# Optimization experiments

Hardware: AMD Instinct MI355X
Metric: run time of the kernel (lower is better)

The kernel has to match this reference:

```python
import jax, jax.numpy as jnp
import numpy as np

N, T, H, E = 16384, 4, 64, 262144
NEG_SLOPE = 0.2  # LeakyReLU slope for GAT-style attention
LN_EPS = 1e-5


def setup_inputs() -> dict:
    key = jax.random.key(0)
    ks = jax.random.split(key, 24)
    p = {}
    p["pred"] = jax.random.normal(ks[0], (N, T, H), jnp.float32)
    p["ei_structural"] = jax.random.randint(ks[1], (2, E), 0, N, jnp.int32)
    p["ei_functional"] = jax.random.randint(ks[2], (2, E), 0, N, jnp.int32)
    scale = 1.0 / np.sqrt(H)
    i = 3
    for l in range(2):
        for et in ("s", "f"):
            p[f"W{l}{et}"] = (jax.random.normal(ks[i], (H, H), jnp.float32) * scale); i += 1
            p[f"a{l}{et}"] = (jax.random.normal(ks[i], (H,), jnp.float32) * scale); i += 1
        p[f"g{l}"] = jnp.ones((H,), jnp.float32)
        p[f"b{l}"] = jnp.zeros((H,), jnp.float32)
    return p


def _conv(x, ei, W, a, n_dst):
    """Attention-based ST graph conv, temporal_kernel_size=1 (per-step)."""
    h = jnp.einsum('nth,hd->ntd', x, W)          # [N,T,H] linear transform
    src, dst = ei[0], ei[1]
    he = h[src]                                   # [E,T,H] gather per edge
    logits = jax.nn.leaky_relu(jnp.einsum('eth,h->et', he, a), NEG_SLOPE)
    m = jax.ops.segment_max(logits, dst, num_segments=n_dst)     # [N,T]
    ex = jnp.exp(logits - m[dst])                 # stable softmax over incoming edges
    den = jax.ops.segment_sum(ex, dst, num_segments=n_dst)
    alpha = ex / den[dst]                         # [E,T]
    return jax.ops.segment_sum(alpha[..., None] * he, dst, num_segments=n_dst)


def _ln(x, g, b):
    mu = x.mean(-1, keepdims=True)
    v = x.var(-1, keepdims=True)
    return (x - mu) * jax.lax.rsqrt(v + LN_EPS) * g + b


def reference(pred, ei_structural, ei_functional,
              W0s, a0s, W0f, a0f, g0, b0,
              W1s, a1s, W1f, a1f, g1, b1):
    x = pred
    layers = ((W0s, a0s, W0f, a0f, g0, b0), (W1s, a1s, W1f, a1f, g1, b1))
    for (Ws, av, Wf, af, g, b) in layers:
        ms = _conv(x, ei_structural, Ws, av, N)
        mf = _conv(x, ei_functional, Wf, af, N)
        # sum(messages)/len(messages), residual, LayerNorm over H (dropout=identity in eval)
        x = _ln(x + 0.5 * (ms + mf), g, b)
    return x
```

## Files before the change

### kernel.cpp

```cpp
#include <hip/hip_runtime.h>
#include <hip/hip_bf16.h>

#define NN 16384
#define TT 4
#define HH 64
#define NT (NN * TT)
#define CAP 128
#define NEG_SLOPE 0.2f
#define LN_EPS 1e-5f

typedef __attribute__((ext_vector_type(8))) short short8;
typedef __attribute__((ext_vector_type(4))) float f32x4;

__device__ __forceinline__ float bf2f(unsigned short u) {
    return __uint_as_float((unsigned)u << 16);
}
__device__ __forceinline__ unsigned short f2bf(float f) {
    unsigned u = __float_as_uint(f);
    return (unsigned short)((u + 0x7FFF + ((u >> 16) & 1)) >> 16);
}


__global__ void zero_kernel(int* __restrict__ a, int n) {
    int i = blockIdx.x * blockDim.x + threadIdx.x;
    if (i < n) a[i] = 0;
}

__global__ void scatter_bucket_kernel(const int* __restrict__ ei_s, const int* __restrict__ ei_f,
                                      int* __restrict__ cnt2, int* __restrict__ col2, int E) {
    int e = blockIdx.x * blockDim.x + threadIdx.x;
    if (e < E) {
        int d = ei_s[E + e];
        int pos = atomicAdd(&cnt2[d], 1);
        if (pos < CAP) col2[d * CAP + pos] = ei_s[e];
    } else {
        e -= E;
        if (e < E) {
            int d = ei_f[E + e];
            int pos = atomicAdd(&cnt2[NN + d], 1);
            if (pos < CAP) col2[(long)NN * CAP + d * CAP + pos] = ei_f[e];
        }
    }
}


__global__ __launch_bounds__(256) void transform2_kernel(
    const float4* __restrict__ x4,
    const float* __restrict__ Ws, const float* __restrict__ as_,
    const float* __restrict__ Wf, const float* __restrict__ af,
    unsigned short* __restrict__ h_s, float* __restrict__ esc_s,
    unsigned short* __restrict__ h_f, float* __restrict__ esc_f) {
    const int lane = threadIdx.x & 63;
    const int wv = threadIdx.x >> 6;
    const int m = lane & 15;
    const int quad = lane >> 4;

    short8 Bs[4][2], Bf[4][2];
#pragma unroll
    for (int c = 0; c < 4; c++) {
#pragma unroll
        for (int ks = 0; ks < 2; ks++) {
#pragma unroll
            for (int j = 0; j < 8; j++) {
                int k = ks * 32 + quad * 8 + j;
                int n = c * 16 + m;
                Bs[c][ks][j] = (short)f2bf(Ws[k * 64 + n]);
                Bf[c][ks][j] = (short)f2bf(Wf[k * 64 + n]);
            }
        }
    }
    float a_s[4], a_f[4];
#pragma unroll
    for (int c = 0; c < 4; c++) { a_s[c] = as_[c * 16 + m]; a_f[c] = af[c * 16 + m]; }

    const int rowbase = blockIdx.x * 128 + wv * 32;
#pragma unroll
    for (int rt = 0; rt < 2; rt++) {
        const int row0 = rowbase + rt * 16;
        const long xbase = (long)(row0 + m) * 16 + quad * 2;
        float4 xa = x4[xbase];
        float4 xb = x4[xbase + 1];
        float4 xc = x4[xbase + 8];
        float4 xd = x4[xbase + 9];
        short8 A0, A1;
        A0[0] = (short)f2bf(xa.x); A0[1] = (short)f2bf(xa.y);
        A0[2] = (short)f2bf(xa.z); A0[3] = (short)f2bf(xa.w);
        A0[4] = (short)f2bf(xb.x); A0[5] = (short)f2bf(xb.y);
        A0[6] = (short)f2bf(xb.z); A0[7] = (short)f2bf(xb.w);
        A1[0] = (short)f2bf(xc.x); A1[1] = (short)f2bf(xc.y);
        A1[2] = (short)f2bf(xc.z); A1[3] = (short)f2bf(xc.w);
        A1[4] = (short)f2bf(xd.x); A1[5] = (short)f2bf(xd.y);
        A1[6] = (short)f2bf(xd.z); A1[7] = (short)f2bf(xd.w);

        f32x4 accs[4], accf[4];
#pragma unroll
        for (int c = 0; c < 4; c++) {
            accs[c] = (f32x4){0.f, 0.f, 0.f, 0.f};
            accf[c] = (f32x4){0.f, 0.f, 0.f, 0.f};
        }
#pragma unroll
        for (int c = 0; c < 4; c++) {
            accs[c] = __builtin_amdgcn_mfma_f32_16x16x32_bf16(A0, Bs[c][0], accs[c], 0, 0, 0);
            accs[c] = __builtin_amdgcn_mfma_f32_16x16x32_bf16(A1, Bs[c][1], accs[c], 0, 0, 0);
            accf[c] = __builtin_amdgcn_mfma_f32_16x16x32_bf16(A0, Bf[c][0], accf[c], 0, 0, 0);
            accf[c] = __builtin_amdgcn_mfma_f32_16x16x32_bf16(A1, Bf[c][1], accf[c], 0, 0, 0);
        }
#pragma unroll
        for (int reg = 0; reg < 4; reg++) {
            const int row = row0 + quad * 4 + reg;
            float ps = 0.f, pf = 0.f;
#pragma unroll
            for (int c = 0; c < 4; c++) {
                h_s[(long)row * 64 + c * 16 + m] = f2bf(accs[c][reg]);
                h_f[(long)row * 64 + c * 16 + m] = f2bf(accf[c][reg]);
                ps = fmaf(accs[c][reg], a_s[c], ps);
                pf = fmaf(accf[c][reg], a_f[c], pf);
            }
#pragma unroll
            for (int off = 1; off < 16; off <<= 1) {
                ps += __shfl_xor(ps, off, 64);
                pf += __shfl_xor(pf, off, 64);
            }
            if (m == 0) {
                float ls = (ps > 0.f) ? ps : NEG_SLOPE * ps;
                float lf = (pf > 0.f) ? pf : NEG_SLOPE * pf;
                esc_s[row] = __expf(ls);
                esc_f[row] = __expf(lf);
            }
        }
    }
}


__global__ __launch_bounds__(256) void aggregate_kernel(
    const float4* __restrict__ x4,
    const ushort4* __restrict__ hs4, const float* __restrict__ escs,
    const int* __restrict__ cnts, const int* __restrict__ cols,
    const ushort4* __restrict__ hf4, const float* __restrict__ escf,
    const int* __restrict__ cntf, const int* __restrict__ colf,
    const float4* __restrict__ g4, const float4* __restrict__ b4,
    float4* __restrict__ out4) {
    const int wv = threadIdx.x >> 6;
    const int lane = threadIdx.x & 63;
    const int n = blockIdx.x * 4 + wv;
    const int t = lane >> 4;
    const int ci = lane & 15;

    int cS = cnts[n]; if (cS > CAP) cS = CAP;
    int cF = cntf[n]; if (cF > CAP) cF = CAP;
    const int* colS = cols + (long)n * CAP;
    const int* colF = colf + (long)n * CAP;

    float dS = 0.f, sx = 0.f, sy = 0.f, sz = 0.f, sw = 0.f;
    float dF = 0.f, fx = 0.f, fy = 0.f, fz = 0.f, fw = 0.f;

    const int nbS = (cS + 3) >> 2;
    const int nbF = (cF + 3) >> 2;
    const int nb = nbS > nbF ? nbS : nbF;

    for (int it = 0; it < nb; ++it) {
        const int j = it << 2;
        const bool doS = it < nbS;
        const bool doF = it < nbF;
        int sS[4], sF[4];
        float eS[4], eF[4];
        ushort4 hS[4], hF[4];

        if (doS) {
#pragma unroll
            for (int u = 0; u < 4; u++) { int idx = j + u; sS[u] = colS[idx < cS ? idx : cS - 1]; }
        }
        if (doF) {
#pragma unroll
            for (int u = 0; u < 4; u++) { int idx = j + u; sF[u] = colF[idx < cF ? idx : cF - 1]; }
        }
        if (doS) {
#pragma unroll
            for (int u = 0; u < 4; u++) { float e = escs[sS[u] * 4 + t]; eS[u] = (j + u < cS) ? e : 0.f; }
#pragma unroll
            for (int u = 0; u < 4; u++) hS[u] = hs4[(long)sS[u] * 64 + lane];
        }
        if (doF) {
#pragma unroll
            for (int u = 0; u < 4; u++) { float e = escf[sF[u] * 4 + t]; eF[u] = (j + u < cF) ? e : 0.f; }
#pragma unroll
            for (int u = 0; u < 4; u++) hF[u] = hf4[(long)sF[u] * 64 + lane];
        }
        if (doS) {
#pragma unroll
            for (int u = 0; u < 4; u++) {
                dS += eS[u];
                sx = fmaf(eS[u], bf2f(hS[u].x), sx);
                sy = fmaf(eS[u], bf2f(hS[u].y), sy);
                sz = fmaf(eS[u], bf2f(hS[u].z), sz);
                sw = fmaf(eS[u], bf2f(hS[u].w), sw);
            }
        }
        if (doF) {
#pragma unroll
            for (int u = 0; u < 4; u++) {
                dF += eF[u];
                fx = fmaf(eF[u], bf2f(hF[u].x), fx);
                fy = fmaf(eF[u], bf2f(hF[u].y), fy);
                fz = fmaf(eF[u], bf2f(hF[u].z), fz);
                fw = fmaf(eF[u], bf2f(hF[u].w), fw);
            }
        }
    }

    float msx = 0.f, msy = 0.f, msz = 0.f, msw = 0.f;
    if (dS > 0.f) {
        float r = 1.f / dS;
        msx = sx * r; msy = sy * r; msz = sz * r; msw = sw * r;
    }
    float mfx = 0.f, mfy = 0.f, mfz = 0.f, mfw = 0.f;
    if (dF > 0.f) {
        float r = 1.f / dF;
        mfx = fx * r; mfy = fy * r; mfz = fz * r; mfw = fw * r;
    }

    float4 xv = x4[(long)n * 64 + lane];
    float v0 = xv.x + 0.5f * (msx + mfx);
    float v1 = xv.y + 0.5f * (msy + mfy);
    float v2 = xv.z + 0.5f * (msz + mfz);
    float v3 = xv.w + 0.5f * (msw + mfw);

    float sum = (v0 + v1) + (v2 + v3);
#pragma unroll
    for (int off = 1; off < 16; off <<= 1) sum += __shfl_xor(sum, off, 64);
    float mu = sum * (1.f / 64.f);
    float d0 = v0 - mu, d1 = v1 - mu, d2 = v2 - mu, d3 = v3 - mu;
    float var = (d0 * d0 + d1 * d1) + (d2 * d2 + d3 * d3);
#pragma unroll
    for (int off = 1; off < 16; off <<= 1) var += __shfl_xor(var, off, 64);
    var *= (1.f / 64.f);
    float inv = rsqrtf(var + LN_EPS);
    float4 gv = g4[ci], bv = b4[ci];
    float4 o;
    o.x = d0 * inv * gv.x + bv.x;
    o.y = d1 * inv * gv.y + bv.y;
    o.z = d2 * inv * gv.z + bv.z;
    o.w = d3 * inv * gv.w + bv.w;
    out4[(long)n * 64 + lane] = o;
}


extern "C" void kernel_launch(void* const* d_in, const int* in_sizes, int n_in,
                              void* d_out, int out_size, void* d_ws, size_t ws_size,
                              hipStream_t stream) {
    const float* pred = (const float*)d_in[0];
    const int* ei_s = (const int*)d_in[1];
    const int* ei_f = (const int*)d_in[2];
    const float* W0s = (const float*)d_in[3];
    const float* a0s = (const float*)d_in[4];
    const float* W0f = (const float*)d_in[5];
    const float* a0f = (const float*)d_in[6];
    const float* g0  = (const float*)d_in[7];
    const float* b0  = (const float*)d_in[8];
    const float* W1s = (const float*)d_in[9];
    const float* a1s = (const float*)d_in[10];
    const float* W1f = (const float*)d_in[11];
    const float* a1f = (const float*)d_in[12];
    const float* g1  = (const float*)d_in[13];
    const float* b1  = (const float*)d_in[14];
    const int E = in_sizes[1] / 2;

    char* ws = (char*)d_ws;
    auto alloc = [&](size_t bytes) {
        char* p = ws;
        ws += (bytes + 255) & ~(size_t)255;
        return p;
    };
    int* cnt2 = (int*)alloc((size_t)2 * NN * sizeof(int));
    int* col2 = (int*)alloc((size_t)2 * NN * CAP * sizeof(int));
    unsigned short* h_s = (unsigned short*)alloc((size_t)NT * HH * sizeof(unsigned short));
    unsigned short* h_f = (unsigned short*)alloc((size_t)NT * HH * sizeof(unsigned short));
    float* esc_s = (float*)alloc((size_t)NT * sizeof(float));
    float* esc_f = (float*)alloc((size_t)NT * sizeof(float));
    float* x_mid = (float*)alloc((size_t)NT * HH * sizeof(float));

    const int* cnt_s = cnt2;
    const int* cnt_f = cnt2 + NN;
    const int* col_s = col2;
    const int* col_f = col2 + (size_t)NN * CAP;

    const int EB = (E + 255) / 256;

    zero_kernel<<<(2 * NN) / 256, 256, 0, stream>>>(cnt2, 2 * NN);
    scatter_bucket_kernel<<<2 * EB, 256, 0, stream>>>(ei_s, ei_f, cnt2, col2, E);

    transform2_kernel<<<NT / 128, 256, 0, stream>>>(
        (const float4*)pred, W0s, a0s, W0f, a0f, h_s, esc_s, h_f, esc_f);
    aggregate_kernel<<<NN / 4, 256, 0, stream>>>(
        (const float4*)pred, (const ushort4*)h_s, esc_s, cnt_s, col_s,
        (const ushort4*)h_f, esc_f, cnt_f, col_f,
        (const float4*)g0, (const float4*)b0, (float4*)x_mid);

    transform2_kernel<<<NT / 128, 256, 0, stream>>>(
        (const float4*)x_mid, W1s, a1s, W1f, a1f, h_s, esc_s, h_f, esc_f);
    aggregate_kernel<<<NN / 4, 256, 0, stream>>>(
        (const float4*)x_mid, (const ushort4*)h_s, esc_s, cnt_s, col_s,
        (const ushort4*)h_f, esc_f, cnt_f, col_f,
        (const float4*)g1, (const float4*)b1, (float4*)d_out);
}
```

Measured before the change: 227.5 us.

## Split neighbor buckets by source half, preload indices per lane, prepack weights

Edge buckets are split four ways (edge type × source-node half) with a capacity of 64 each. The aggregate kernel loads one wave-wide vector of neighbor indices per bucket and broadcasts them with readlane, instead of issuing scalar column loads inside the loop. Gathers are unrolled by 8 and grouped so each phase touches only half of the h table, which may improve cache locality. Weights are also converted to bf16 MFMA fragments once in a small prepack kernel rather than in every transform block. The trade-off is an extra launch, more count and column storage, and a tighter per-bucket cap that could drop edges for skewed graphs.

```diff
diff --git a/kernel.cpp b/kernel.cpp
--- a/kernel.cpp
+++ b/kernel.cpp
@@ -5,7 +5,7 @@
 #define TT 4
 #define HH 64
 #define NT (NN * TT)
-#define CAP 128
+#define CAPH 64
 #define NEG_SLOPE 0.2f
 #define LN_EPS 1e-5f
 
@@ -26,28 +26,51 @@
     if (i < n) a[i] = 0;
 }
 
-__global__ void scatter_bucket_kernel(const int* __restrict__ ei_s, const int* __restrict__ ei_f,
-                                      int* __restrict__ cnt2, int* __restrict__ col2, int E) {
+__global__ void scatter4_kernel(const int* __restrict__ ei_s, const int* __restrict__ ei_f,
+                                int* __restrict__ cnt4, int* __restrict__ col4, int E) {
     int e = blockIdx.x * blockDim.x + threadIdx.x;
+    int src, d, set;
     if (e < E) {
-        int d = ei_s[E + e];
-        int pos = atomicAdd(&cnt2[d], 1);
-        if (pos < CAP) col2[d * CAP + pos] = ei_s[e];
+        set = 0; src = ei_s[e]; d = ei_s[E + e];
     } else {
         e -= E;
-        if (e < E) {
-            int d = ei_f[E + e];
-            int pos = atomicAdd(&cnt2[NN + d], 1);
-            if (pos < CAP) col2[(long)NN * CAP + d * CAP + pos] = ei_f[e];
-        }
-    }
+        if (e >= E) return;
+        set = 1; src = ei_f[e]; d = ei_f[E + e];
+    }
+    int half = src >> 13;
+    int p = set * 2 + half;
+    int pos = atomicAdd(&cnt4[p * NN + d], 1);
+    if (pos < CAPH) col4[((long)p * NN + d) * CAPH + pos] = src;
+}
+
+
+__global__ __launch_bounds__(256) void packw_kernel(
+    const float* __restrict__ W0s_, const float* __restrict__ W0f_,
+    const float* __restrict__ W1s_, const float* __restrict__ W1f_,
+    short8* __restrict__ wpack) {
+    int id = blockIdx.x * 256 + threadIdx.x;
+    int mat = id >> 9;
+    int slot = id & 511;
+    int lane = slot & 63;
+    int cks = slot >> 6;
+    int c = cks >> 1, ks = cks & 1;
+    int m = lane & 15, quad = lane >> 4;
+    const float* W = (mat == 0) ? W0s_ : (mat == 1) ? W0f_ : (mat == 2) ? W1s_ : W1f_;
+    short8 v;
+#pragma unroll
+    for (int j = 0; j < 8; j++) {
+        int k = ks * 32 + quad * 8 + j;
+        int n = c * 16 + m;
+        v[j] = (short)f2bf(W[k * 64 + n]);
+    }
+    wpack[id] = v;
 }
 
 
 __global__ __launch_bounds__(256) void transform2_kernel(
     const float4* __restrict__ x4,
-    const float* __restrict__ Ws, const float* __restrict__ as_,
-    const float* __restrict__ Wf, const float* __restrict__ af,
+    const short8* __restrict__ wp_s, const float* __restrict__ as_,
+    const short8* __restrict__ wp_f, const float* __restrict__ af,
     unsigned short* __restrict__ h_s, float* __restrict__ esc_s,
     unsigned short* __restrict__ h_f, float* __restrict__ esc_f) {
     const int lane = threadIdx.x & 63;
@@ -60,13 +83,8 @@
     for (int c = 0; c < 4; c++) {
 #pragma unroll
         for (int ks = 0; ks < 2; ks++) {
-#pragma unroll
-            for (int j = 0; j < 8; j++) {
-                int k = ks * 32 + quad * 8 + j;
-                int n = c * 16 + m;
-                Bs[c][ks][j] = (short)f2bf(Ws[k * 64 + n]);
-                Bf[c][ks][j] = (short)f2bf(Wf[k * 64 + n]);
-            }
+            Bs[c][ks] = wp_s[(c * 2 + ks) * 64 + lane];
+            Bf[c][ks] = wp_f[(c * 2 + ks) * 64 + lane];
         }
     }
     float a_s[4], a_f[4];
@@ -132,12 +150,40 @@
 }
 
 
+__device__ __forceinline__ void agg_phase(const ushort4* __restrict__ h4,
+                                          const float* __restrict__ esc,
+                                          int idx, int c, int t, int lane,
+                                          float& den, float& ax, float& ay,
+                                          float& az, float& aw) {
+    const int nb = (c + 7) >> 3;
+    for (int it = 0; it < nb; ++it) {
+        const int j = it << 3;
+        int s[8];
+        float e[8];
+        ushort4 h[8];
+#pragma unroll
+        for (int u = 0; u < 8; u++) s[u] = __builtin_amdgcn_readlane(idx, j + u);
+#pragma unroll
+        for (int u = 0; u < 8; u++) h[u] = h4[s[u] * 64 + lane];
+#pragma unroll
+        for (int u = 0; u < 8; u++) e[u] = esc[s[u] * 4 + t];
+#pragma unroll
+        for (int u = 0; u < 8; u++) {
+            float w = (j + u < c) ? e[u] : 0.f;
+            den += w;
+            ax = fmaf(w, bf2f(h[u].x), ax);
+            ay = fmaf(w, bf2f(h[u].y), ay);
+            az = fmaf(w, bf2f(h[u].z), az);
+            aw = fmaf(w, bf2f(h[u].w), aw);
+        }
+    }
+}
+
 __global__ __launch_bounds__(256) void aggregate_kernel(
     const float4* __restrict__ x4,
     const ushort4* __restrict__ hs4, const float* __restrict__ escs,
-    const int* __restrict__ cnts, const int* __restrict__ cols,
     const ushort4* __restrict__ hf4, const float* __restrict__ escf,
-    const int* __restrict__ cntf, const int* __restrict__ colf,
+    const int* __restrict__ cnt4, const int* __restrict__ col4,
     const float4* __restrict__ g4, const float4* __restrict__ b4,
     float4* __restrict__ out4) {
     const int wv = threadIdx.x >> 6;
@@ -146,67 +192,23 @@
     const int t = lane >> 4;
     const int ci = lane & 15;
 
-    int cS = cnts[n]; if (cS > CAP) cS = CAP;
-    int cF = cntf[n]; if (cF > CAP) cF = CAP;
-    const int* colS = cols + (long)n * CAP;
-    const int* colF = colf + (long)n * CAP;
+    int cc[4], idx[4];
+#pragma unroll
+    for (int p = 0; p < 4; p++) {
+        int cv = cnt4[p * NN + n];
+        if (cv > CAPH) cv = CAPH;
+        cc[p] = __builtin_amdgcn_readfirstlane(cv);
+        idx[p] = col4[((long)p * NN + n) * CAPH + lane];
+        if (lane >= cc[p]) idx[p] = 0;
+    }
 
     float dS = 0.f, sx = 0.f, sy = 0.f, sz = 0.f, sw = 0.f;
     float dF = 0.f, fx = 0.f, fy = 0.f, fz = 0.f, fw = 0.f;
 
-    const int nbS = (cS + 3) >> 2;
-    const int nbF = (cF + 3) >> 2;
-    const int nb = nbS > nbF ? nbS : nbF;
-
-    for (int it = 0; it < nb; ++it) {
-        const int j = it << 2;
-        const bool doS = it < nbS;
-        const bool doF = it < nbF;
-        int sS[4], sF[4];
-        float eS[4], eF[4];
-        ushort4 hS[4], hF[4];
-
-        if (doS) {
-#pragma unroll
-            for (int u = 0; u < 4; u++) { int idx = j + u; sS[u] = colS[idx < cS ? idx : cS - 1]; }
-        }
-        if (doF) {
-#pragma unroll
-            for (int u = 0; u < 4; u++) { int idx = j + u; sF[u] = colF[idx < cF ? idx : cF - 1]; }
-        }
-        if (doS) {
-#pragma unroll
-            for (int u = 0; u < 4; u++) { float e = escs[sS[u] * 4 + t]; eS[u] = (j + u < cS) ? e : 0.f; }
-#pragma unroll
-            for (int u = 0; u < 4; u++) hS[u] = hs4[(long)sS[u] * 64 + lane];
-        }
-        if (doF) {
-#pragma unroll
-            for (int u = 0; u < 4; u++) { float e = escf[sF[u] * 4 + t]; eF[u] = (j + u < cF) ? e : 0.f; }
-#pragma unroll
-            for (int u = 0; u < 4; u++) hF[u] = hf4[(long)sF[u] * 64 + lane];
-        }
-        if (doS) {
-#pragma unroll
-            for (int u = 0; u < 4; u++) {
-                dS += eS[u];
-                sx = fmaf(eS[u], bf2f(hS[u].x), sx);
-                sy = fmaf(eS[u], bf2f(hS[u].y), sy);
-                sz = fmaf(eS[u], bf2f(hS[u].z), sz);
-                sw = fmaf(eS[u], bf2f(hS[u].w), sw);
-            }
-        }
-        if (doF) {
-#pragma unroll
-            for (int u = 0; u < 4; u++) {
-                dF += eF[u];
-                fx = fmaf(eF[u], bf2f(hF[u].x), fx);
-                fy = fmaf(eF[u], bf2f(hF[u].y), fy);
-                fz = fmaf(eF[u], bf2f(hF[u].z), fz);
-                fw = fmaf(eF[u], bf2f(hF[u].w), fw);
-            }
-        }
-    }
+    agg_phase(hs4, escs, idx[0], cc[0], t, lane, dS, sx, sy, sz, sw);
+    agg_phase(hs4, escs, idx[1], cc[1], t, lane, dS, sx, sy, sz, sw);
+    agg_phase(hf4, escf, idx[2], cc[2], t, lane, dF, fx, fy, fz, fw);
+    agg_phase(hf4, escf, idx[3], cc[3], t, lane, dF, fx, fy, fz, fw);
 
     float msx = 0.f, msy = 0.f, msz = 0.f, msw = 0.f;
     if (dS > 0.f) {
@@ -271,35 +273,33 @@
         ws += (bytes + 255) & ~(size_t)255;
         return p;
     };
-    int* cnt2 = (int*)alloc((size_t)2 * NN * sizeof(int));
-    int* col2 = (int*)alloc((size_t)2 * NN * CAP * sizeof(int));
+    int* cnt4 = (int*)alloc((size_t)4 * NN * sizeof(int));
+    int* col4 = (int*)alloc((size_t)4 * NN * CAPH * sizeof(int));
+    short8* wpack = (short8*)alloc((size_t)4 * 512 * sizeof(short8));
     unsigned short* h_s = (unsigned short*)alloc((size_t)NT * HH * sizeof(unsigned short));
     unsigned short* h_f = (unsigned short*)alloc((size_t)NT * HH * sizeof(unsigned short));
     float* esc_s = (float*)alloc((size_t)NT * sizeof(float));
     float* esc_f = (float*)alloc((size_t)NT * sizeof(float));
     float* x_mid = (float*)alloc((size_t)NT * HH * sizeof(float));
 
-    const int* cnt_s = cnt2;
-    const int* cnt_f = cnt2 + NN;
-    const int* col_s = col2;
-    const int* col_f = col2 + (size_t)NN * CAP;
-
     const int EB = (E + 255) / 256;
 
-    zero_kernel<<<(2 * NN) / 256, 256, 0, stream>>>(cnt2, 2 * NN);
-    scatter_bucket_kernel<<<2 * EB, 256, 0, stream>>>(ei_s, ei_f, cnt2, col2, E);
+    packw_kernel<<<8, 256, 0, stream>>>(W0s, W0f, W1s, W1f, wpack);
+
+    zero_kernel<<<(4 * NN) / 256, 256, 0, stream>>>(cnt4, 4 * NN);
+    scatter4_kernel<<<2 * EB, 256, 0, stream>>>(ei_s, ei_f, cnt4, col4, E);
 
     transform2_kernel<<<NT / 128, 256, 0, stream>>>(
-        (const float4*)pred, W0s, a0s, W0f, a0f, h_s, esc_s, h_f, esc_f);
+        (const float4*)pred, wpack, a0s, wpack + 512, a0f, h_s, esc_s, h_f, esc_f);
     aggregate_kernel<<<NN / 4, 256, 0, stream>>>(
-        (const float4*)pred, (const ushort4*)h_s, esc_s, cnt_s, col_s,
-        (const ushort4*)h_f, esc_f, cnt_f, col_f,
+        (const float4*)pred, (const ushort4*)h_s, esc_s,
+        (const ushort4*)h_f, esc_f, cnt4, col4,
         (const float4*)g0, (const float4*)b0, (float4*)x_mid);
 
     transform2_kernel<<<NT / 128, 256, 0, stream>>>(
-        (const float4*)x_mid, W1s, a1s, W1f, a1f, h_s, esc_s, h_f, esc_f);
+        (const float4*)x_mid, wpack + 1024, a1s, wpack + 1536, a1f, h_s, esc_s, h_f, esc_f);
     aggregate_kernel<<<NN / 4, 256, 0, stream>>>(
-        (const float4*)x_mid, (const ushort4*)h_s, esc_s, cnt_s, col_s,
-        (const ushort4*)h_f, esc_f, cnt_f, col_f,
+        (const float4*)x_mid, (const ushort4*)h_s, esc_s,
+        (const ushort4*)h_f, esc_f, cnt4, col4,
         (const float4*)g1, (const float4*)b1, (float4*)d_out);
 }
```

Result: no change. 229.7 us (+0.9%).
